# Optimization experiments

Measured on AMD Instinct MI355X. Metric: run time of the kernel, lower is better.

The kernel has to match this reference:

```python
import jax, jax.numpy as jnp
import numpy as np

EMBED_DIM = 1024
N_HEADS = 16
HEAD_DIM = EMBED_DIM // N_HEADS


def setup_inputs() -> dict:
    key = jax.random.key(0)
    ks = jax.random.split(key, 6)
    B, S, D = 4, 2048, EMBED_DIM
    s = 1.0 / np.sqrt(D)
    return {
        "x": jax.random.normal(ks[0], (B, S, D), dtype=jnp.float32),
        "Wq": jax.random.normal(ks[1], (D, D), dtype=jnp.float32) * s,
        "Wk": jax.random.normal(ks[2], (D, D), dtype=jnp.float32) * s,
        "Wv": jax.random.normal(ks[3], (D, D), dtype=jnp.float32) * s,
        "Wo": jax.random.normal(ks[4], (D, D), dtype=jnp.float32) * s,
        "bo": jax.random.normal(ks[5], (D,), dtype=jnp.float32) * 0.01,
    }


def reference(x, Wq, Wk, Wv, Wo, bo):
    B, S, D = x.shape
    H, Hd = N_HEADS, HEAD_DIM
    # q,k,v: [B,S,D] -> [B,H,S,Hd]
    def proj(W):
        return (x @ W.T).reshape(B, S, H, Hd).transpose(0, 2, 1, 3)
    q, k, v = proj(Wq), proj(Wk), proj(Wv)
    scores = jnp.einsum("bhqd,bhkd->bhqk", q, k) / jnp.sqrt(jnp.float32(Hd))
    attn = jax.nn.softmax(scores, axis=-1)  # dropout p=0.0 -> identity
    out = jnp.einsum("bhqk,bhkd->bhqd", attn, v)  # [B,H,S,Hd]
    out = out.transpose(0, 2, 1, 3).reshape(B, S, D)
    return out @ Wo.T + bo
```

## Files before the change

kernel.cpp:

```cpp
#include <hip/hip_runtime.h>


typedef unsigned short u16;
typedef unsigned int u32;
typedef float f32x4 __attribute__((ext_vector_type(4)));
typedef float f32x16 __attribute__((ext_vector_type(16)));
typedef short s16x8 __attribute__((ext_vector_type(8)));

#define DEVI __device__ __forceinline__

DEVI u16 f32_bf16(float f) {
  unsigned u = __float_as_uint(f);
  return (u16)((u + 0x7FFFu + ((u >> 16) & 1u)) >> 16);
}

DEVI u32 pack_pk(float a, float b) {
  u32 r;
  asm("v_cvt_pk_bf16_f32 %0, %1, %2" : "=v"(r) : "v"(a), "v"(b));
  return r;
}

DEVI void gload_lds16(const void* g, void* l) {
  __builtin_amdgcn_global_load_lds((const __attribute__((address_space(1))) void*)g,
                                   (__attribute__((address_space(3))) void*)l, 16, 0, 0);
}

#if __has_builtin(__builtin_amdgcn_permlane32_swap)
typedef int i32x2 __attribute__((ext_vector_type(2)));
DEVI void plswap(u32& a, u32& b, int hi) {
  i32x2 r = __builtin_amdgcn_permlane32_swap((int)a, (int)b, false, false);
  a = (u32)r[0];
  b = (u32)r[1];
}
#else
DEVI void plswap(u32& a, u32& b, int hi) {
  u32 ta = (u32)__shfl_xor((int)a, 32);
  u32 tb = (u32)__shfl_xor((int)b, 32);
  u32 na = hi ? tb : a;
  u32 nb = hi ? b : ta;
  a = na;
  b = nb;
}
#endif

__global__ void cvt_kernel(const float* __restrict__ in, u16* __restrict__ out, int n4) {
  int i = blockIdx.x * 256 + threadIdx.x;
  if (i >= n4) return;
  float4 v = ((const float4*)in)[i];
  ushort4 o;
  o.x = f32_bf16(v.x); o.y = f32_bf16(v.y);
  o.z = f32_bf16(v.z); o.w = f32_bf16(v.w);
  ((ushort4*)out)[i] = o;
}

__global__ void cvt_w_kernel(const float* __restrict__ wq, const float* __restrict__ wk,
                             const float* __restrict__ wv, const float* __restrict__ wo,
                             u16* __restrict__ wcat, u16* __restrict__ wo_bf) {
  int i = blockIdx.x * 256 + threadIdx.x;
  int m = blockIdx.y;
  const float* src = (m == 0) ? wq : (m == 1) ? wk : (m == 2) ? wv : wo;
  u16* dst = (m < 3) ? (wcat + m * 1048576) : wo_bf;
  float4 v = ((const float4*)src)[i];
  ushort4 o;
  o.x = f32_bf16(v.x); o.y = f32_bf16(v.y);
  o.z = f32_bf16(v.z); o.w = f32_bf16(v.w);
  ((ushort4*)dst)[i] = o;
}

template <int MODE>
__global__ __launch_bounds__(256, 3) void gemm_bt(
    const u16* __restrict__ A, const u16* __restrict__ B, void* __restrict__ Cout,
    const float* __restrict__ bias, int M, int N, int K) {
  __shared__ u16 As[128 * 64];
  __shared__ u16 Bs[128 * 64];
  const int tid = threadIdx.x;
  const int lane = tid & 63;
  const int w = tid >> 6;
  const int wr = w >> 1, wc = w & 1;
  const int l15 = lane & 15, l4 = lane >> 4;
  const int swz = (l15 & 7) << 3;

  const int gx = gridDim.x;
  const int nwg = gx * gridDim.y;
  int ib = blockIdx.y * gx + blockIdx.x;
  int t = (ib & 7) * (nwg >> 3) + (ib >> 3);
  const int m0 = (t / gx) * 128, n0 = (t % gx) * 128;

  const int srow = w * 8 + (lane >> 3);
  const int scol = ((lane & 7) ^ (lane >> 3)) * 8;

  f32x4 acc[4][4] = {};

  for (int k0 = 0; k0 < K; k0 += 64) {
    __syncthreads();
#pragma unroll
    for (int i = 0; i < 4; ++i) {
      int cb = i * 256 + w * 64;
      int r = i * 32 + srow;
      gload_lds16(A + (size_t)(m0 + r) * K + k0 + scol, &As[cb * 8]);
      gload_lds16(B + (size_t)(n0 + r) * K + k0 + scol, &Bs[cb * 8]);
    }
    __syncthreads();

    s16x8 af[4][2], bf[4][2];
#pragma unroll
    for (int m = 0; m < 4; ++m)
#pragma unroll
      for (int ks = 0; ks < 2; ++ks)
        af[m][ks] = *(const s16x8*)&As[(wr * 64 + m * 16 + l15) * 64 +
                                       ((ks * 32 + l4 * 8) ^ swz)];
#pragma unroll
    for (int n = 0; n < 4; ++n)
#pragma unroll
      for (int ks = 0; ks < 2; ++ks)
        bf[n][ks] = *(const s16x8*)&Bs[(wc * 64 + n * 16 + l15) * 64 +
                                       ((ks * 32 + l4 * 8) ^ swz)];
    __builtin_amdgcn_s_setprio(1);
#pragma unroll
    for (int m = 0; m < 4; ++m)
#pragma unroll
      for (int n = 0; n < 4; ++n)
#pragma unroll
        for (int ks = 0; ks < 2; ++ks)
          acc[m][n] = __builtin_amdgcn_mfma_f32_16x16x32_bf16(af[m][ks], bf[n][ks],
                                                              acc[m][n], 0, 0, 0);
    __builtin_amdgcn_s_setprio(0);
  }

#pragma unroll
  for (int m = 0; m < 4; ++m) {
    int row = m0 + wr * 64 + m * 16 + l4 * 4;
#pragma unroll
    for (int n = 0; n < 4; ++n) {
      int col = n0 + wc * 64 + n * 16 + l15;
      if (MODE == 0) {
        u16* C = (u16*)Cout;
        float scale = (col < 1024) ? 0.18033688f : 1.0f;
#pragma unroll
        for (int j = 0; j < 4; ++j)
          C[(size_t)(row + j) * N + col] = f32_bf16(acc[m][n][j] * scale);
      } else {
        float* C = (float*)Cout;
        float bb = bias[col];
#pragma unroll
        for (int j = 0; j < 4; ++j)
          C[(size_t)(row + j) * N + col] = acc[m][n][j] + bb;
      }
    }
  }
}

__global__ __launch_bounds__(256, 4) void attn_kernel(const u16* __restrict__ QKV,
                                                      u16* __restrict__ AO) {
  __shared__ u16 Ks[2][64 * 64];
  __shared__ u16 Vt[2][64 * 64];
  const int tid = threadIdx.x;
  const int lane = tid & 63, w = tid >> 6;
  const int l31 = lane & 31, hi = lane >> 5;

  int ib = blockIdx.z * 256 + blockIdx.y * 16 + blockIdx.x;
  int tb = (ib & 7) * 128 + (ib >> 3);
  const int h = (tb >> 4) & 15, b = tb >> 8;
  const int rowbase = b * 2048;
  const int q0 = (tb & 15) * 128 + w * 32;

  s16x8 qa[4];
  {
    const u16* qp = QKV + (size_t)(rowbase + q0 + l31) * 3072 + h * 64 + hi * 8;
#pragma unroll
    for (int s = 0; s < 4; ++s) qa[s] = *(const s16x8*)(qp + s * 16);
  }

  const char* kbase = (const char*)(QKV + (size_t)rowbase * 3072 + 1024 + h * 64);
  const u16* vbase = QKV + (size_t)rowbase * 3072 + 2048 + h * 64;

  const int kgrow = lane >> 3;
  const int kgcol = ((lane & 7) * 16) ^ ((lane >> 3) << 4);
  const int kv = (tid & 31) * 2;
  const int dv = (tid >> 5) * 8;

  f32x16 o0 = {}, o1 = {};
  float mrow = -1e30f, lrow = 0.f;

  {
#pragma unroll
    for (int c = 0; c < 2; ++c) {
      int chunk = w * 2 + c;
      gload_lds16(kbase + (chunk * 8 + kgrow) * 6144 + kgcol, &Ks[0][chunk * 512]);
    }
    const u16* vp = vbase + kv * 3072 + dv;
    s16x8 v0 = *(const s16x8*)vp, v1 = *(const s16x8*)(vp + 3072);
#pragma unroll
    for (int i = 0; i < 8; ++i) {
      int d = dv + i;
      *(u32*)((char*)&Vt[0][0] + d * 128 + ((kv * 2) ^ ((d & 7) << 4))) =
          (u32)(u16)v0[i] | ((u32)(u16)v1[i] << 16);
    }
  }
  __syncthreads();

  for (int kt = 0; kt < 32; ++kt) {
    const int cur = kt & 1;
    if (kt < 31) {
      const char* kb = kbase + (size_t)(kt + 1) * 64 * 6144;
#pragma unroll
      for (int c = 0; c < 2; ++c) {
        int chunk = w * 2 + c;
        gload_lds16(kb + (chunk * 8 + kgrow) * 6144 + kgcol, &Ks[cur ^ 1][chunk * 512]);
      }
    }

    const char* Kb = (const char*)&Ks[cur][0];
    const char* Vb = (const char*)&Vt[cur][0];
    s16x8 v0, v1;

#pragma unroll
    for (int step = 0; step < 2; ++step) {
      const int keyrow = step * 32 + l31;
      const int swzk = (keyrow & 7) << 4;
      f32x16 s_acc = {};
      __builtin_amdgcn_s_setprio(1);
#pragma unroll
      for (int s = 0; s < 4; ++s) {
        s16x8 kf = *(const s16x8*)(Kb + keyrow * 128 + ((s * 32 + hi * 16) ^ swzk));
        s_acc = __builtin_amdgcn_mfma_f32_32x32x16_bf16(kf, qa[s], s_acc, 0, 0, 0);
      }
      __builtin_amdgcn_s_setprio(0);

      float mx[8];
#pragma unroll
      for (int r = 0; r < 8; ++r) mx[r] = fmaxf(s_acc[r], s_acc[r + 8]);
#pragma unroll
      for (int r = 0; r < 4; ++r) mx[r] = fmaxf(mx[r], mx[r + 4]);
      float m4 = fmaxf(fmaxf(mx[0], mx[1]), fmaxf(mx[2], mx[3]));
      m4 = fmaxf(m4, __shfl_xor(m4, 32));
      if (!__all(m4 <= mrow + 8.f)) {
        float mnew = fmaxf(mrow, m4);
        float corr = __builtin_amdgcn_exp2f(mrow - mnew);
        lrow *= corr;
#pragma unroll
        for (int r = 0; r < 16; ++r) { o0[r] *= corr; o1[r] *= corr; }
        mrow = mnew;
      }
      u32 pk[8];
      float s0 = 0.f, s1 = 0.f, s2 = 0.f, s3 = 0.f;
#pragma unroll
      for (int j = 0; j < 8; ++j) {
        float a = __builtin_amdgcn_exp2f(s_acc[2 * j] - mrow);
        float c = __builtin_amdgcn_exp2f(s_acc[2 * j + 1] - mrow);
        pk[j] = pack_pk(a, c);
        if ((j & 3) == 0) s0 += a + c;
        else if ((j & 3) == 1) s1 += a + c;
        else if ((j & 3) == 2) s2 += a + c;
        else s3 += a + c;
      }
      float rs = (s0 + s1) + (s2 + s3);
      rs += __shfl_xor(rs, 32);
      lrow += rs;

      plswap(pk[0], pk[2], hi);
      plswap(pk[1], pk[3], hi);
      plswap(pk[4], pk[6], hi);
      plswap(pk[5], pk[7], hi);
      union { u32 u[4]; s16x8 v; } pb0, pb1;
      pb0.u[0] = pk[0]; pb0.u[1] = pk[1]; pb0.u[2] = pk[2]; pb0.u[3] = pk[3];
      pb1.u[0] = pk[4]; pb1.u[1] = pk[5]; pb1.u[2] = pk[6]; pb1.u[3] = pk[7];

      const int swzv = (l31 & 7) << 4;
      __builtin_amdgcn_s_setprio(1);
#pragma unroll
      for (int ks = 0; ks < 2; ++ks) {
        int cbyte = (step * 64 + ks * 32 + hi * 16) ^ swzv;
        s16x8 vf0 = *(const s16x8*)(Vb + l31 * 128 + cbyte);
        s16x8 vf1 = *(const s16x8*)(Vb + (32 + l31) * 128 + cbyte);
        s16x8 pf = ks ? pb1.v : pb0.v;
        o0 = __builtin_amdgcn_mfma_f32_32x32x16_bf16(vf0, pf, o0, 0, 0, 0);
        o1 = __builtin_amdgcn_mfma_f32_32x32x16_bf16(vf1, pf, o1, 0, 0, 0);
      }
      __builtin_amdgcn_s_setprio(0);

      if (step == 0 && kt < 31) {
        const u16* vp = vbase + ((kt + 1) * 64 + kv) * 3072 + dv;
        v0 = *(const s16x8*)vp;
        v1 = *(const s16x8*)(vp + 3072);
      }
    }

    if (kt < 31) {
#pragma unroll
      for (int i = 0; i < 8; ++i) {
        int d = dv + i;
        *(u32*)((char*)&Vt[cur ^ 1][0] + d * 128 + ((kv * 2) ^ ((d & 7) << 4))) =
            (u32)(u16)v0[i] | ((u32)(u16)v1[i] << 16);
      }
    }
    __syncthreads();
  }

  float inv = __builtin_amdgcn_rcpf(lrow);
  u16* op = AO + (size_t)(rowbase + q0 + l31) * 1024 + h * 64;
#pragma unroll
  for (int g = 0; g < 4; ++g) {
    ushort4 s0, s1;
    s0.x = f32_bf16(o0[g * 4 + 0] * inv);
    s0.y = f32_bf16(o0[g * 4 + 1] * inv);
    s0.z = f32_bf16(o0[g * 4 + 2] * inv);
    s0.w = f32_bf16(o0[g * 4 + 3] * inv);
    s1.x = f32_bf16(o1[g * 4 + 0] * inv);
    s1.y = f32_bf16(o1[g * 4 + 1] * inv);
    s1.z = f32_bf16(o1[g * 4 + 2] * inv);
    s1.w = f32_bf16(o1[g * 4 + 3] * inv);
    *(ushort4*)(op + g * 8 + 4 * hi) = s0;
    *(ushort4*)(op + 32 + g * 8 + 4 * hi) = s1;
  }
}

extern "C" void kernel_launch(void* const* d_in, const int* in_sizes, int n_in,
                              void* d_out, int out_size, void* d_ws, size_t ws_size,
                              hipStream_t stream) {
  const float* x = (const float*)d_in[0];
  const float* Wq = (const float*)d_in[1];
  const float* Wk = (const float*)d_in[2];
  const float* Wv = (const float*)d_in[3];
  const float* Wo = (const float*)d_in[4];
  const float* bo = (const float*)d_in[5];
  float* out = (float*)d_out;

  char* ws = (char*)d_ws;
  u16* x_bf = (u16*)ws;
  u16* Wcat = (u16*)(ws + 16777216);
  u16* Wo_bf = (u16*)(ws + 16777216 + 6291456);
  u16* QKV = (u16*)(ws + 16777216 + 6291456 + 2097152);
  u16* AO = (u16*)(ws + 16777216 + 6291456 + 2097152 + 50331648);

  cvt_kernel<<<8192, 256, 0, stream>>>(x, x_bf, 8192 * 1024 / 4);
  cvt_w_kernel<<<dim3(1024, 4), 256, 0, stream>>>(Wq, Wk, Wv, Wo, Wcat, Wo_bf);

  gemm_bt<0><<<dim3(24, 64), 256, 0, stream>>>(x_bf, Wcat, QKV, nullptr, 8192, 3072, 1024);
  attn_kernel<<<dim3(16, 16, 4), 256, 0, stream>>>(QKV, AO);
  gemm_bt<1><<<dim3(8, 64), 256, 0, stream>>>(AO, Wo_bf, out, bo, 8192, 1024, 1024);
}
```

Baseline: 204.0 us.

## Enlarge attention tiles to 256 queries and 128-key blocks with 8 waves

The attention kernel now runs 512 threads per block covering 256 query rows, and streams K/V in 128-key tiles so there are half as many iterations and barriers. Each K/V tile in LDS is shared by twice as many waves, which cuts global K/V traffic per query. QK^T for two 32-key subtiles is issued back to back before the softmax work, and the cross-half max and sum reductions use permlane32_swap instead of shuffles. LDS use doubles to 64KB per block, and the larger blocks may lower occupancy and leave fewer blocks to spread across CUs.

```diff
diff --git a/kernel.cpp b/kernel.cpp
--- a/kernel.cpp
+++ b/kernel.cpp
@@ -31,6 +31,16 @@
   i32x2 r = __builtin_amdgcn_permlane32_swap((int)a, (int)b, false, false);
   a = (u32)r[0];
   b = (u32)r[1];
+}
+DEVI float xhalf_max(float x) {
+  i32x2 r = __builtin_amdgcn_permlane32_swap(__float_as_int(x), __float_as_int(x),
+                                             false, false);
+  return fmaxf(__int_as_float(r[0]), __int_as_float(r[1]));
+}
+DEVI float xhalf_add(float x) {
+  i32x2 r = __builtin_amdgcn_permlane32_swap(__float_as_int(x), __float_as_int(x),
+                                             false, false);
+  return __int_as_float(r[0]) + __int_as_float(r[1]);
 }
 #else
 DEVI void plswap(u32& a, u32& b, int hi) {
@@ -41,6 +51,8 @@
   a = na;
   b = nb;
 }
+DEVI float xhalf_max(float x) { return fmaxf(x, __shfl_xor(x, 32)); }
+DEVI float xhalf_add(float x) { return x + __shfl_xor(x, 32); }
 #endif
 
 __global__ void cvt_kernel(const float* __restrict__ in, u16* __restrict__ out, int n4) {
@@ -150,19 +162,19 @@
   }
 }
 
-__global__ __launch_bounds__(256, 4) void attn_kernel(const u16* __restrict__ QKV,
+__global__ __launch_bounds__(512, 4) void attn_kernel(const u16* __restrict__ QKV,
                                                       u16* __restrict__ AO) {
-  __shared__ u16 Ks[2][64 * 64];
-  __shared__ u16 Vt[2][64 * 64];
+  __shared__ u16 Ks[2][128 * 64];
+  __shared__ u16 Vt[2][64 * 128];
   const int tid = threadIdx.x;
   const int lane = tid & 63, w = tid >> 6;
   const int l31 = lane & 31, hi = lane >> 5;
 
-  int ib = blockIdx.z * 256 + blockIdx.y * 16 + blockIdx.x;
-  int tb = (ib & 7) * 128 + (ib >> 3);
-  const int h = (tb >> 4) & 15, b = tb >> 8;
+  int ib = blockIdx.z * 128 + blockIdx.y * 8 + blockIdx.x;
+  int tb = (ib & 7) * 64 + (ib >> 3);
+  const int h = (tb >> 3) & 15, b = tb >> 7;
   const int rowbase = b * 2048;
-  const int q0 = (tb & 15) * 128 + w * 32;
+  const int q0 = (tb & 7) * 256 + w * 32;
 
   s16x8 qa[4];
   {
@@ -176,8 +188,10 @@
 
   const int kgrow = lane >> 3;
   const int kgcol = ((lane & 7) * 16) ^ ((lane >> 3) << 4);
-  const int kv = (tid & 31) * 2;
-  const int dv = (tid >> 5) * 8;
+  const int kv = lane * 2;
+  const int dv = w * 8;
+
+  const int swzr = (l31 & 7) << 4;
 
   f32x16 o0 = {}, o1 = {};
   float mrow = -1e30f, lrow = 0.f;
@@ -193,16 +207,16 @@
 #pragma unroll
     for (int i = 0; i < 8; ++i) {
       int d = dv + i;
-      *(u32*)((char*)&Vt[0][0] + d * 128 + ((kv * 2) ^ ((d & 7) << 4))) =
+      *(u32*)((char*)&Vt[0][0] + d * 256 + ((kv * 2) ^ ((d & 7) << 4))) =
           (u32)(u16)v0[i] | ((u32)(u16)v1[i] << 16);
     }
   }
   __syncthreads();
 
-  for (int kt = 0; kt < 32; ++kt) {
+  for (int kt = 0; kt < 16; ++kt) {
     const int cur = kt & 1;
-    if (kt < 31) {
-      const char* kb = kbase + (size_t)(kt + 1) * 64 * 6144;
+    if (kt < 15) {
+      const char* kb = kbase + (size_t)(kt + 1) * 128 * 6144;
 #pragma unroll
       for (int c = 0; c < 2; ++c) {
         int chunk = w * 2 + c;
@@ -215,82 +229,89 @@
     s16x8 v0, v1;
 
 #pragma unroll
-    for (int step = 0; step < 2; ++step) {
-      const int keyrow = step * 32 + l31;
-      const int swzk = (keyrow & 7) << 4;
-      f32x16 s_acc = {};
+    for (int sp = 0; sp < 2; ++sp) {
+      f32x16 sa0 = {}, sa1 = {};
       __builtin_amdgcn_s_setprio(1);
 #pragma unroll
       for (int s = 0; s < 4; ++s) {
-        s16x8 kf = *(const s16x8*)(Kb + keyrow * 128 + ((s * 32 + hi * 16) ^ swzk));
-        s_acc = __builtin_amdgcn_mfma_f32_32x32x16_bf16(kf, qa[s], s_acc, 0, 0, 0);
+        s16x8 kf = *(const s16x8*)(Kb + (sp * 64 + l31) * 128 + ((s * 32 + hi * 16) ^ swzr));
+        sa0 = __builtin_amdgcn_mfma_f32_32x32x16_bf16(kf, qa[s], sa0, 0, 0, 0);
+      }
+#pragma unroll
+      for (int s = 0; s < 4; ++s) {
+        s16x8 kf = *(const s16x8*)(Kb + (sp * 64 + 32 + l31) * 128 + ((s * 32 + hi * 16) ^ swzr));
+        sa1 = __builtin_amdgcn_mfma_f32_32x32x16_bf16(kf, qa[s], sa1, 0, 0, 0);
       }
       __builtin_amdgcn_s_setprio(0);
 
-      float mx[8];
-#pragma unroll
-      for (int r = 0; r < 8; ++r) mx[r] = fmaxf(s_acc[r], s_acc[r + 8]);
-#pragma unroll
-      for (int r = 0; r < 4; ++r) mx[r] = fmaxf(mx[r], mx[r + 4]);
-      float m4 = fmaxf(fmaxf(mx[0], mx[1]), fmaxf(mx[2], mx[3]));
-      m4 = fmaxf(m4, __shfl_xor(m4, 32));
-      if (!__all(m4 <= mrow + 8.f)) {
-        float mnew = fmaxf(mrow, m4);
-        float corr = __builtin_amdgcn_exp2f(mrow - mnew);
-        lrow *= corr;
-#pragma unroll
-        for (int r = 0; r < 16; ++r) { o0[r] *= corr; o1[r] *= corr; }
-        mrow = mnew;
-      }
-      u32 pk[8];
-      float s0 = 0.f, s1 = 0.f, s2 = 0.f, s3 = 0.f;
-#pragma unroll
-      for (int j = 0; j < 8; ++j) {
-        float a = __builtin_amdgcn_exp2f(s_acc[2 * j] - mrow);
-        float c = __builtin_amdgcn_exp2f(s_acc[2 * j + 1] - mrow);
-        pk[j] = pack_pk(a, c);
-        if ((j & 3) == 0) s0 += a + c;
-        else if ((j & 3) == 1) s1 += a + c;
-        else if ((j & 3) == 2) s2 += a + c;
-        else s3 += a + c;
-      }
-      float rs = (s0 + s1) + (s2 + s3);
-      rs += __shfl_xor(rs, 32);
-      lrow += rs;
-
-      plswap(pk[0], pk[2], hi);
-      plswap(pk[1], pk[3], hi);
-      plswap(pk[4], pk[6], hi);
-      plswap(pk[5], pk[7], hi);
-      union { u32 u[4]; s16x8 v; } pb0, pb1;
-      pb0.u[0] = pk[0]; pb0.u[1] = pk[1]; pb0.u[2] = pk[2]; pb0.u[3] = pk[3];
-      pb1.u[0] = pk[4]; pb1.u[1] = pk[5]; pb1.u[2] = pk[6]; pb1.u[3] = pk[7];
-
-      const int swzv = (l31 & 7) << 4;
-      __builtin_amdgcn_s_setprio(1);
-#pragma unroll
-      for (int ks = 0; ks < 2; ++ks) {
-        int cbyte = (step * 64 + ks * 32 + hi * 16) ^ swzv;
-        s16x8 vf0 = *(const s16x8*)(Vb + l31 * 128 + cbyte);
-        s16x8 vf1 = *(const s16x8*)(Vb + (32 + l31) * 128 + cbyte);
-        s16x8 pf = ks ? pb1.v : pb0.v;
-        o0 = __builtin_amdgcn_mfma_f32_32x32x16_bf16(vf0, pf, o0, 0, 0, 0);
-        o1 = __builtin_amdgcn_mfma_f32_32x32x16_bf16(vf1, pf, o1, 0, 0, 0);
-      }
-      __builtin_amdgcn_s_setprio(0);
-
-      if (step == 0 && kt < 31) {
-        const u16* vp = vbase + ((kt + 1) * 64 + kv) * 3072 + dv;
+#pragma unroll
+      for (int sub = 0; sub < 2; ++sub) {
+        const int st = sp * 2 + sub;
+        f32x16 s_acc = sub ? sa1 : sa0;
+
+        float a0 = fmaxf(fmaxf(s_acc[0], s_acc[1]), s_acc[2]);
+        float a1 = fmaxf(fmaxf(s_acc[3], s_acc[4]), s_acc[5]);
+        float a2 = fmaxf(fmaxf(s_acc[6], s_acc[7]), s_acc[8]);
+        float a3 = fmaxf(fmaxf(s_acc[9], s_acc[10]), s_acc[11]);
+        float a4 = fmaxf(fmaxf(s_acc[12], s_acc[13]), s_acc[14]);
+        float m4 = fmaxf(fmaxf(fmaxf(a0, a1), a2),
+                         fmaxf(fmaxf(a3, a4), s_acc[15]));
+        m4 = xhalf_max(m4);
+        if (!__all(m4 <= mrow + 8.f)) {
+          float mnew = fmaxf(mrow, m4);
+          float corr = __builtin_amdgcn_exp2f(mrow - mnew);
+          lrow *= corr;
+#pragma unroll
+          for (int r = 0; r < 16; ++r) { o0[r] *= corr; o1[r] *= corr; }
+          mrow = mnew;
+        }
+        u32 pk[8];
+        float s0 = 0.f, s1 = 0.f, s2 = 0.f, s3 = 0.f;
+#pragma unroll
+        for (int j = 0; j < 8; ++j) {
+          float a = __builtin_amdgcn_exp2f(s_acc[2 * j] - mrow);
+          float c = __builtin_amdgcn_exp2f(s_acc[2 * j + 1] - mrow);
+          pk[j] = pack_pk(a, c);
+          if ((j & 3) == 0) s0 += a + c;
+          else if ((j & 3) == 1) s1 += a + c;
+          else if ((j & 3) == 2) s2 += a + c;
+          else s3 += a + c;
+        }
+        lrow += xhalf_add((s0 + s1) + (s2 + s3));
+
+        plswap(pk[0], pk[2], hi);
+        plswap(pk[1], pk[3], hi);
+        plswap(pk[4], pk[6], hi);
+        plswap(pk[5], pk[7], hi);
+        union { u32 u[4]; s16x8 v; } pb0, pb1;
+        pb0.u[0] = pk[0]; pb0.u[1] = pk[1]; pb0.u[2] = pk[2]; pb0.u[3] = pk[3];
+        pb1.u[0] = pk[4]; pb1.u[1] = pk[5]; pb1.u[2] = pk[6]; pb1.u[3] = pk[7];
+
+        __builtin_amdgcn_s_setprio(1);
+#pragma unroll
+        for (int ks = 0; ks < 2; ++ks) {
+          int cbyte = (st * 64 + ks * 32 + hi * 16) ^ swzr;
+          s16x8 vf0 = *(const s16x8*)(Vb + l31 * 256 + cbyte);
+          s16x8 vf1 = *(const s16x8*)(Vb + (32 + l31) * 256 + cbyte);
+          s16x8 pf = ks ? pb1.v : pb0.v;
+          o0 = __builtin_amdgcn_mfma_f32_32x32x16_bf16(vf0, pf, o0, 0, 0, 0);
+          o1 = __builtin_amdgcn_mfma_f32_32x32x16_bf16(vf1, pf, o1, 0, 0, 0);
+        }
+        __builtin_amdgcn_s_setprio(0);
+      }
+
+      if (sp == 0 && kt < 15) {
+        const u16* vp = vbase + ((kt + 1) * 128 + kv) * 3072 + dv;
         v0 = *(const s16x8*)vp;
         v1 = *(const s16x8*)(vp + 3072);
       }
     }
 
-    if (kt < 31) {
+    if (kt < 15) {
 #pragma unroll
       for (int i = 0; i < 8; ++i) {
         int d = dv + i;
-        *(u32*)((char*)&Vt[cur ^ 1][0] + d * 128 + ((kv * 2) ^ ((d & 7) << 4))) =
+        *(u32*)((char*)&Vt[cur ^ 1][0] + d * 256 + ((kv * 2) ^ ((d & 7) << 4))) =
             (u32)(u16)v0[i] | ((u32)(u16)v1[i] << 16);
       }
     }
@@ -337,6 +358,6 @@
   cvt_w_kernel<<<dim3(1024, 4), 256, 0, stream>>>(Wq, Wk, Wv, Wo, Wcat, Wo_bf);
 
   gemm_bt<0><<<dim3(24, 64), 256, 0, stream>>>(x_bf, Wcat, QKV, nullptr, 8192, 3072, 1024);
-  attn_kernel<<<dim3(16, 16, 4), 256, 0, stream>>>(QKV, AO);
+  attn_kernel<<<dim3(8, 16, 4), 512, 0, stream>>>(QKV, AO);
   gemm_bt<1><<<dim3(8, 64), 256, 0, stream>>>(AO, Wo_bf, out, bo, 8192, 1024, 1024);
 }
```

Measured after the change: 196.3 us. 3.8% less time.
